# Kernel optimization log

Measured on AMD Instinct MI355X. Metric: run time of the kernel, lower is better.

## Reference

```python
import jax, jax.numpy as jnp
import numpy as np

NUM_LAYERS = 3
DROPOUT_P = 0.1


def _spmm(rows, cols, vals, X, num_rows):
    # COO SpMM: out[r] = sum_{e: rows[e]==r} vals[e] * X[cols[e]]
    return jax.ops.segment_sum(vals[:, None] * X[cols], rows, num_segments=num_rows)


def setup_inputs() -> dict:
    key = jax.random.key(0)
    ks = jax.random.split(key, 8)
    N, H, D, NNZ = 50000, 50000, 256, 1600000
    poi_embs = jax.random.normal(ks[0], (N, D), dtype=jnp.float32)
    src_row = jax.random.randint(ks[1], (NNZ,), 0, N, dtype=jnp.int32)
    src_col = jax.random.randint(ks[2], (NNZ,), 0, H, dtype=jnp.int32)
    src_val = jax.random.uniform(ks[3], (NNZ,), dtype=jnp.float32)
    tar_row = jax.random.randint(ks[4], (NNZ,), 0, H, dtype=jnp.int32)
    tar_col = jax.random.randint(ks[5], (NNZ,), 0, N, dtype=jnp.int32)
    tar_val = jax.random.uniform(ks[6], (NNZ,), dtype=jnp.float32)
    return {
        "poi_embs": poi_embs,
        "src_row": src_row, "src_col": src_col, "src_val": src_val,
        "tar_row": tar_row, "tar_col": tar_col, "tar_val": tar_val,
        "num_pois": N, "num_hyperedges": H,
    }


def reference(poi_embs, src_row, src_col, src_val, tar_row, tar_col, tar_val,
              num_pois, num_hyperedges):
    keep = 1.0 - DROPOUT_P
    drop_key = jax.random.key(42)
    finals = [poi_embs]  # [N, D]
    x = poi_embs
    for i in range(NUM_LAYERS):
        msg_tar = _spmm(tar_row, tar_col, tar_val, x, num_hyperedges)   # [H, D]
        msg_src = _spmm(src_row, src_col, src_val, msg_tar, num_pois)   # [N, D]
        h = msg_src + finals[-1]
        mask = jax.random.bernoulli(jax.random.fold_in(drop_key, i), keep, h.shape)
        x = jnp.where(mask, h / keep, 0.0)  # inverted dropout, training=True
        finals.append(x)
    return jnp.mean(jnp.stack(finals), axis=0)
```

## Files before the change

### kernel.cpp

```cpp
#include <hip/hip_runtime.h>
#include <hip/hip_fp16.h>
#include <stdint.h>

#define DD 256
#define BK_SHIFT 10
#define NB 98
#define CHUNK 4096

typedef float    fx4 __attribute__((ext_vector_type(4)));
typedef uint32_t ux2 __attribute__((ext_vector_type(2)));

__host__ __device__ __forceinline__ uint32_t rotl32(uint32_t v, int r) {
  return (v << r) | (v >> (32 - r));
}

__host__ __device__ inline void tf2x32(uint32_t k0, uint32_t k1,
                                       uint32_t& x0, uint32_t& x1) {
  uint32_t ks0 = k0, ks1 = k1, ks2 = k0 ^ k1 ^ 0x1BD11BDAu;
  x0 += ks0; x1 += ks1;
#define TF_RND(r) { x0 += x1; x1 = rotl32(x1, (r)); x1 ^= x0; }
  TF_RND(13) TF_RND(15) TF_RND(26) TF_RND(6)
  x0 += ks1; x1 += ks2 + 1u;
  TF_RND(17) TF_RND(29) TF_RND(16) TF_RND(24)
  x0 += ks2; x1 += ks0 + 2u;
  TF_RND(13) TF_RND(15) TF_RND(26) TF_RND(6)
  x0 += ks0; x1 += ks1 + 3u;
  TF_RND(17) TF_RND(29) TF_RND(16) TF_RND(24)
  x0 += ks1; x1 += ks2 + 4u;
  TF_RND(13) TF_RND(15) TF_RND(26) TF_RND(6)
  x0 += ks2; x1 += ks0 + 5u;
#undef TF_RND
}

__device__ __forceinline__ float2 h2f(uint32_t u) {
  __half2 h = *(__half2*)&u;
  return __half22float2(h);
}

__global__ void init_kernel(const float* __restrict__ p, uint32_t* __restrict__ xh,
                            float* __restrict__ out, int total4) {
  int t4 = blockIdx.x * blockDim.x + threadIdx.x;
  if (t4 >= total4) return;
  fx4 v = __builtin_nontemporal_load((const fx4*)p + t4);
  __builtin_nontemporal_store(v, (fx4*)out + t4);
  __half2 h0 = __floats2half2_rn(v.x, v.y);
  __half2 h1 = __floats2half2_rn(v.z, v.w);
  ux2 u;
  u.x = *(const uint32_t*)&h0;
  u.y = *(const uint32_t*)&h1;
  __builtin_nontemporal_store(u, (ux2*)xh + t4);
}

__global__ __launch_bounds__(256) void bucket_hist(
    const int* __restrict__ t_row, int nnz_t,
    const int* __restrict__ s_row, int nnz_s,
    int* __restrict__ gbcnt, int H) {
  __shared__ int lcnt[NB];
  for (int i = threadIdx.x; i < NB; i += 256) lcnt[i] = 0;
  __syncthreads();
  const int base = blockIdx.x * CHUNK;
  const int nnz_all = nnz_t + nnz_s;
#pragma unroll
  for (int k = 0; k < CHUNK / 256; ++k) {
    int e = base + k * 256 + threadIdx.x;
    if (e < nnz_all) {
      int slot = (e < nnz_t) ? t_row[e] : (H + s_row[e - nnz_t]);
      atomicAdd(&lcnt[slot >> BK_SHIFT], 1);
    }
  }
  __syncthreads();
  for (int i = threadIdx.x; i < NB; i += 256)
    if (lcnt[i]) atomicAdd(&gbcnt[i], lcnt[i]);
}

__global__ void bucket_scan(const int* __restrict__ gbcnt,
                            int* __restrict__ bbase, int* __restrict__ gcur) {
  if (threadIdx.x == 0) {
    int run = 0;
    for (int i = 0; i < NB; ++i) { bbase[i] = run; gcur[i] = run; run += gbcnt[i]; }
    bbase[NB] = run;
  }
}

__global__ __launch_bounds__(256) void coarse_scatter(
    const int* __restrict__ t_row, const int* __restrict__ t_col,
    const float* __restrict__ t_val, int nnz_t,
    const int* __restrict__ s_row, const int* __restrict__ s_col,
    const float* __restrict__ s_val, int nnz_s,
    int* __restrict__ gcur, uint64_t* __restrict__ staging, int H) {
  __shared__ int lcnt[NB], lbase[NB], gofs[NB];
  __shared__ int ltotal;
  __shared__ uint64_t stage[CHUNK];
  const int tid = threadIdx.x;
  for (int i = tid; i < NB; i += 256) lcnt[i] = 0;
  __syncthreads();
  const int base = blockIdx.x * CHUNK;
  const int nnz_all = nnz_t + nnz_s;
  uint64_t rec[CHUNK / 256];
#pragma unroll
  for (int k = 0; k < CHUNK / 256; ++k) {
    int e = base + k * 256 + tid;
    if (e < nnz_all) {
      int slot, col; float val;
      if (e < nnz_t) { slot = t_row[e]; col = t_col[e]; val = t_val[e]; }
      else { int i2 = e - nnz_t; slot = H + s_row[i2]; col = s_col[i2]; val = s_val[i2]; }
      uint32_t packed = ((uint32_t)col << 16) |
                        (uint32_t)__half_as_ushort(__float2half_rn(val));
      rec[k] = ((uint64_t)(uint32_t)slot << 32) | packed;
      atomicAdd(&lcnt[slot >> BK_SHIFT], 1);
    } else {
      rec[k] = ~0ull;
    }
  }
  __syncthreads();
  if (tid == 0) {
    int run = 0;
    for (int i = 0; i < NB; ++i) { lbase[i] = run; run += lcnt[i]; }
    ltotal = run;
  }
  __syncthreads();
  if (tid < NB) {
    if (lcnt[tid]) gofs[tid] = atomicAdd(&gcur[tid], lcnt[tid]);
    lcnt[tid] = 0;
  }
  __syncthreads();
#pragma unroll
  for (int k = 0; k < CHUNK / 256; ++k) {
    int slot = (int)(rec[k] >> 32);
    if (slot >= 0) {
      int b = slot >> BK_SHIFT;
      int p = atomicAdd(&lcnt[b], 1);
      stage[lbase[b] + p] = rec[k];
    }
  }
  __syncthreads();
  const int tot = ltotal;
  for (int i = tid; i < tot; i += 256) {
    uint64_t r = stage[i];
    int b = (int)(r >> 32) >> BK_SHIFT;
    staging[(size_t)gofs[b] + (i - lbase[b])] = r;
  }
}

__global__ __launch_bounds__(256) void fine_scatter(
    const uint64_t* __restrict__ staging, const int* __restrict__ bbase,
    int* __restrict__ offs, uint32_t* __restrict__ epk, int slots) {
  __shared__ int scnt[1024];
  __shared__ int sofs[1024];
  __shared__ int wsum[4];
  const int b = blockIdx.x;
  const int bb = bbase[b], be = bbase[b + 1];
  const int tid = threadIdx.x;
  for (int i = tid; i < 1024; i += 256) scnt[i] = 0;
  __syncthreads();
  for (int i = bb + tid; i < be; i += 256)
    atomicAdd(&scnt[(int)(staging[i] >> 32) & 1023], 1);
  __syncthreads();
  const int base4 = tid * 4;
  int v[4], pre[4];
#pragma unroll
  for (int k = 0; k < 4; ++k) v[k] = scnt[base4 + k];
  int tsum = 0;
#pragma unroll
  for (int k = 0; k < 4; ++k) { pre[k] = tsum; tsum += v[k]; }
  int lane = tid & 63, wv = tid >> 6;
  int inc = tsum;
  for (int off = 1; off < 64; off <<= 1) {
    int up = __shfl_up(inc, off, 64);
    if (lane >= off) inc += up;
  }
  if (lane == 63) wsum[wv] = inc;
  __syncthreads();
  int wbase = 0;
  for (int w = 0; w < wv; ++w) wbase += wsum[w];
  int texc = wbase + inc - tsum;
#pragma unroll
  for (int k = 0; k < 4; ++k) sofs[base4 + k] = texc + pre[k];
  __syncthreads();
#pragma unroll
  for (int k = 0; k < 4; ++k) {
    int g = (b << BK_SHIFT) + base4 + k;
    if (g < slots) offs[g] = bb + sofs[base4 + k] + v[k];
  }
  __syncthreads();
  for (int i = bb + tid; i < be; i += 256) {
    uint64_t r = staging[i];
    int ls = (int)(r >> 32) & 1023;
    int p = atomicAdd(&sofs[ls], 1);
    epk[(size_t)bb + p] = (uint32_t)r;
  }
}

#define GATHER_BODY(SRC)                                                          \
  float4 acc = make_float4(0.f, 0.f, 0.f, 0.f);                                   \
  int i = b;                                                                      \
  for (; i + 7 < e; i += 8) {                                                     \
    uint32_t E[8]; uint2 A[8];                                                    \
    _Pragma("unroll")                                                             \
    for (int k = 0; k < 8; ++k) E[k] = __builtin_nontemporal_load(ep + i + k);    \
    _Pragma("unroll")                                                             \
    for (int k = 0; k < 8; ++k) A[k] = SRC[(size_t)(E[k] >> 16) * 64 + lane];     \
    _Pragma("unroll")                                                             \
    for (int k = 0; k < 8; ++k) {                                                 \
      float v = __half2float(__ushort_as_half((unsigned short)(E[k] & 0xFFFFu))); \
      float2 f0 = h2f(A[k].x), f1 = h2f(A[k].y);                                  \
      acc.x += v * f0.x; acc.y += v * f0.y;                                       \
      acc.z += v * f1.x; acc.w += v * f1.y;                                       \
    }                                                                             \
  }                                                                               \
  for (; i < e; ++i) {                                                            \
    uint32_t E0 = __builtin_nontemporal_load(ep + i);                             \
    uint2 A0 = SRC[(size_t)(E0 >> 16) * 64 + lane];                               \
    float v = __half2float(__ushort_as_half((unsigned short)(E0 & 0xFFFFu)));     \
    float2 f0 = h2f(A0.x), f1 = h2f(A0.y);                                        \
    acc.x += v * f0.x; acc.y += v * f0.y;                                         \
    acc.z += v * f1.x; acc.w += v * f1.y;                                         \
  }

__global__ __launch_bounds__(256) void spmm_full(
    const int* __restrict__ offs, const uint32_t* __restrict__ ep,
    const uint2* __restrict__ X, uint2* __restrict__ Y, int nrows, int grow_base) {
  int wid = threadIdx.x >> 6, lane = threadIdx.x & 63;
  int r = blockIdx.x * 4 + wid;
  if (r >= nrows) return;
  int g = grow_base + r;
  int b = (g == 0) ? 0 : offs[g - 1];
  int e = offs[g];
  GATHER_BODY(X)
  __half2 o0 = __floats2half2_rn(acc.x, acc.y);
  __half2 o1 = __floats2half2_rn(acc.z, acc.w);
  uint2 o;
  o.x = *(const uint32_t*)&o0;
  o.y = *(const uint32_t*)&o1;
  Y[(size_t)r * 64 + lane] = o;
}

__global__ __launch_bounds__(256) void spmm_drop_full(
    const int* __restrict__ offs, const uint32_t* __restrict__ ep,
    const uint2* __restrict__ T, uint2* __restrict__ x, float* __restrict__ out,
    uint32_t k0, uint32_t k1, int nrows, int grow_base, int is_final) {
  int wid = threadIdx.x >> 6, lane = threadIdx.x & 63;
  int r = blockIdx.x * 4 + wid;
  if (r >= nrows) return;
  int g = grow_base + r;
  int b = (g == 0) ? 0 : offs[g - 1];
  int e = offs[g];
  GATHER_BODY(T)
  size_t xi = (size_t)r * 64 + lane;
  ux2 xv_u = __builtin_nontemporal_load((const ux2*)x + xi);
  float2 x0 = h2f(xv_u.x), x1 = h2f(xv_u.y);
  float h[4] = {acc.x + x0.x, acc.y + x0.y, acc.z + x1.x, acc.w + x1.y};
  int j0 = r * DD + lane * 4;
  float xn[4];
#pragma unroll
  for (int k = 0; k < 4; ++k) {
    uint32_t r0 = 0u, r1 = (uint32_t)(j0 + k);
    tf2x32(k0, k1, r0, r1);
    uint32_t bits = r0 ^ r1;
    float u = __uint_as_float((bits >> 9) | 0x3f800000u) - 1.0f;
    xn[k] = (u < 0.9f) ? h[k] * (1.0f / 0.9f) : 0.0f;
  }
  __half2 nx0 = __floats2half2_rn(xn[0], xn[1]);
  __half2 nx1 = __floats2half2_rn(xn[2], xn[3]);
  ux2 nxu;
  nxu.x = *(const uint32_t*)&nx0;
  nxu.y = *(const uint32_t*)&nx1;
  __builtin_nontemporal_store(nxu, (ux2*)x + xi);
  fx4 ov = __builtin_nontemporal_load((const fx4*)out + xi);
  ov.x += xn[0]; ov.y += xn[1]; ov.z += xn[2]; ov.w += xn[3];
  if (is_final) { ov.x *= 0.25f; ov.y *= 0.25f; ov.z *= 0.25f; ov.w *= 0.25f; }
  __builtin_nontemporal_store(ov, (fx4*)out + xi);
}

extern "C" void kernel_launch(void* const* d_in, const int* in_sizes, int n_in,
                              void* d_out, int out_size, void* d_ws, size_t ws_size,
                              hipStream_t stream) {
  const float* p     = (const float*)d_in[0];
  const int*   s_row = (const int*)d_in[1];
  const int*   s_col = (const int*)d_in[2];
  const float* s_val = (const float*)d_in[3];
  const int*   t_row = (const int*)d_in[4];
  const int*   t_col = (const int*)d_in[5];
  const float* t_val = (const float*)d_in[6];

  const int nnz_s = in_sizes[1];
  const int nnz_t = in_sizes[4];
  const int N = in_sizes[0] / DD;
  const int H = 50000;
  const int slots = H + N;
  const int nnz_all = nnz_t + nnz_s;

  uint2*    xh      = (uint2*)d_ws;
  uint2*    th      = xh + (size_t)N * 64;
  uint64_t* staging = (uint64_t*)(th + (size_t)H * 64);
  uint32_t* epk     = (uint32_t*)(staging + nnz_all);
  int*      offs    = (int*)(epk + nnz_all);
  int*      gbcnt   = offs + slots;
  int*      bbase   = gbcnt + NB;
  int*      gcur    = bbase + (NB + 1);

  float* out = (float*)d_out;

  (void)hipMemsetAsync(gbcnt, 0, sizeof(int) * NB, stream);
  const int cblocks = (nnz_all + CHUNK - 1) / CHUNK;
  bucket_hist<<<cblocks, 256, 0, stream>>>(t_row, nnz_t, s_row, nnz_s, gbcnt, H);
  bucket_scan<<<1, 64, 0, stream>>>(gbcnt, bbase, gcur);
  coarse_scatter<<<cblocks, 256, 0, stream>>>(t_row, t_col, t_val, nnz_t,
                                              s_row, s_col, s_val, nnz_s,
                                              gcur, staging, H);
  fine_scatter<<<NB, 256, 0, stream>>>(staging, bbase, offs, epk, slots);

  const int total4 = N * DD / 4;
  init_kernel<<<(total4 + 255) / 256, 256, 0, stream>>>(p, (uint32_t*)xh, out, total4);

  for (int i = 0; i < 3; ++i) {
    spmm_full<<<(H + 3) / 4, 256, 0, stream>>>(offs, epk, xh, th, H, 0);
    uint32_t x0 = 0u, x1 = (uint32_t)i;
    tf2x32(0u, 42u, x0, x1);
    spmm_drop_full<<<(N + 3) / 4, 256, 0, stream>>>(offs, epk, th, xh, out,
                                                    x0, x1, N, H, i == 2);
  }
}
```

Baseline: 854.2 us.

## Bin edges by column range and gather in phases for cache locality

The fine scatter now sorts each row's edges into 16 column-range bins, using 4096-column ranges, and records per-bin offsets. The SpMM kernels loop over 13 column phases, with each wave handling 9 rows, so concurrently running waves tend to touch the same slice of the source matrix and reuse it from L2. The running fp32 output accumulation is removed: layer outputs go to separate fp16 buffers, and the final kernel computes the mean once, with one buffer reusing the staging area. The cost is a 16x larger offset table, more offset loads and short segments per row, and fp16 rounding of the intermediate layers used in the mean.

```diff
diff --git a/kernel.cpp b/kernel.cpp
--- a/kernel.cpp
+++ b/kernel.cpp
@@ -3,9 +3,16 @@
 #include <stdint.h>
 
 #define DD 256
-#define BK_SHIFT 10
-#define NB 98
+#define BK_SHIFT 9
+#define SLOTS_PER_BK 512
+#define NB 196
 #define CHUNK 4096
+#define CSHIFT 12
+#define NPH 13
+#define BPS 16
+#define RPW 9
+#define WPB 8
+#define RPB (RPW * WPB)
 
 typedef float    fx4 __attribute__((ext_vector_type(4)));
 typedef uint32_t ux2 __attribute__((ext_vector_type(2)));
@@ -38,11 +45,10 @@
 }
 
 __global__ void init_kernel(const float* __restrict__ p, uint32_t* __restrict__ xh,
-                            float* __restrict__ out, int total4) {
+                            int total4) {
   int t4 = blockIdx.x * blockDim.x + threadIdx.x;
   if (t4 >= total4) return;
   fx4 v = __builtin_nontemporal_load((const fx4*)p + t4);
-  __builtin_nontemporal_store(v, (fx4*)out + t4);
   __half2 h0 = __floats2half2_rn(v.x, v.y);
   __half2 h1 = __floats2half2_rn(v.z, v.w);
   ux2 u;
@@ -144,25 +150,27 @@
 
 __global__ __launch_bounds__(256) void fine_scatter(
     const uint64_t* __restrict__ staging, const int* __restrict__ bbase,
-    int* __restrict__ offs, uint32_t* __restrict__ epk, int slots) {
-  __shared__ int scnt[1024];
-  __shared__ int sofs[1024];
+    int* __restrict__ boffs, uint32_t* __restrict__ epk, int slots) {
+  __shared__ int scnt[SLOTS_PER_BK * BPS];
+  __shared__ int sofs[SLOTS_PER_BK * BPS];
   __shared__ int wsum[4];
   const int b = blockIdx.x;
   const int bb = bbase[b], be = bbase[b + 1];
   const int tid = threadIdx.x;
-  for (int i = tid; i < 1024; i += 256) scnt[i] = 0;
-  __syncthreads();
-  for (int i = bb + tid; i < be; i += 256)
-    atomicAdd(&scnt[(int)(staging[i] >> 32) & 1023], 1);
-  __syncthreads();
-  const int base4 = tid * 4;
-  int v[4], pre[4];
-#pragma unroll
-  for (int k = 0; k < 4; ++k) v[k] = scnt[base4 + k];
+  for (int i = tid; i < SLOTS_PER_BK * BPS; i += 256) scnt[i] = 0;
+  __syncthreads();
+  for (int i = bb + tid; i < be; i += 256) {
+    uint64_t r = staging[i];
+    int slot = (int)(r >> 32);
+    int col = (int)(((uint32_t)r) >> 16);
+    int bin = ((slot & (SLOTS_PER_BK - 1)) << 4) | (col >> CSHIFT);
+    atomicAdd(&scnt[bin], 1);
+  }
+  __syncthreads();
+  const int base32 = tid * 32;
   int tsum = 0;
 #pragma unroll
-  for (int k = 0; k < 4; ++k) { pre[k] = tsum; tsum += v[k]; }
+  for (int k = 0; k < 32; ++k) tsum += scnt[base32 + k];
   int lane = tid & 63, wv = tid >> 6;
   int inc = tsum;
   for (int off = 1; off < 64; off <<= 1) {
@@ -173,103 +181,168 @@
   __syncthreads();
   int wbase = 0;
   for (int w = 0; w < wv; ++w) wbase += wsum[w];
-  int texc = wbase + inc - tsum;
-#pragma unroll
-  for (int k = 0; k < 4; ++k) sofs[base4 + k] = texc + pre[k];
-  __syncthreads();
-#pragma unroll
-  for (int k = 0; k < 4; ++k) {
-    int g = (b << BK_SHIFT) + base4 + k;
-    if (g < slots) offs[g] = bb + sofs[base4 + k] + v[k];
+  int run = wbase + inc - tsum;
+#pragma unroll
+  for (int k = 0; k < 32; ++k) { int v = scnt[base32 + k]; sofs[base32 + k] = run; run += v; }
+  __syncthreads();
+  const int gb0 = b * (SLOTS_PER_BK * BPS);
+  const int nbins_total = slots * BPS;
+  for (int i = tid; i < SLOTS_PER_BK * BPS; i += 256) {
+    int g = gb0 + i;
+    if (g < nbins_total) boffs[g] = bb + sofs[i];
   }
   __syncthreads();
   for (int i = bb + tid; i < be; i += 256) {
     uint64_t r = staging[i];
-    int ls = (int)(r >> 32) & 1023;
-    int p = atomicAdd(&sofs[ls], 1);
-    epk[(size_t)bb + p] = (uint32_t)r;
-  }
-}
-
-#define GATHER_BODY(SRC)                                                          \
-  float4 acc = make_float4(0.f, 0.f, 0.f, 0.f);                                   \
-  int i = b;                                                                      \
-  for (; i + 7 < e; i += 8) {                                                     \
-    uint32_t E[8]; uint2 A[8];                                                    \
+    int slot = (int)(r >> 32);
+    uint32_t packed = (uint32_t)r;
+    int bin = ((slot & (SLOTS_PER_BK - 1)) << 4) | ((int)(packed >> 16) >> CSHIFT);
+    int p = atomicAdd(&sofs[bin], 1);
+    epk[(size_t)bb + p] = packed;
+  }
+}
+
+#define SEG_GATHER(SRC, ACC)                                                      \
+  {                                                                               \
+    int i = sb;                                                                   \
+    for (; i + 3 < se; i += 4) {                                                  \
+      uint32_t E0 = __builtin_nontemporal_load(ep + i);                           \
+      uint32_t E1 = __builtin_nontemporal_load(ep + i + 1);                       \
+      uint32_t E2 = __builtin_nontemporal_load(ep + i + 2);                       \
+      uint32_t E3 = __builtin_nontemporal_load(ep + i + 3);                       \
+      uint2 A0 = SRC[(size_t)(E0 >> 16) * 64 + lane];                             \
+      uint2 A1 = SRC[(size_t)(E1 >> 16) * 64 + lane];                             \
+      uint2 A2 = SRC[(size_t)(E2 >> 16) * 64 + lane];                             \
+      uint2 A3 = SRC[(size_t)(E3 >> 16) * 64 + lane];                             \
+      float v0 = __half2float(__ushort_as_half((unsigned short)(E0 & 0xFFFFu)));  \
+      float v1 = __half2float(__ushort_as_half((unsigned short)(E1 & 0xFFFFu)));  \
+      float v2 = __half2float(__ushort_as_half((unsigned short)(E2 & 0xFFFFu)));  \
+      float v3 = __half2float(__ushort_as_half((unsigned short)(E3 & 0xFFFFu)));  \
+      float2 f0, f1;                                                              \
+      f0 = h2f(A0.x); f1 = h2f(A0.y);                                             \
+      ACC.x += v0 * f0.x; ACC.y += v0 * f0.y; ACC.z += v0 * f1.x; ACC.w += v0 * f1.y; \
+      f0 = h2f(A1.x); f1 = h2f(A1.y);                                             \
+      ACC.x += v1 * f0.x; ACC.y += v1 * f0.y; ACC.z += v1 * f1.x; ACC.w += v1 * f1.y; \
+      f0 = h2f(A2.x); f1 = h2f(A2.y);                                             \
+      ACC.x += v2 * f0.x; ACC.y += v2 * f0.y; ACC.z += v2 * f1.x; ACC.w += v2 * f1.y; \
+      f0 = h2f(A3.x); f1 = h2f(A3.y);                                             \
+      ACC.x += v3 * f0.x; ACC.y += v3 * f0.y; ACC.z += v3 * f1.x; ACC.w += v3 * f1.y; \
+    }                                                                             \
+    for (; i < se; ++i) {                                                         \
+      uint32_t E0 = __builtin_nontemporal_load(ep + i);                           \
+      uint2 A0 = SRC[(size_t)(E0 >> 16) * 64 + lane];                             \
+      float v0 = __half2float(__ushort_as_half((unsigned short)(E0 & 0xFFFFu)));  \
+      float2 f0 = h2f(A0.x), f1 = h2f(A0.y);                                      \
+      ACC.x += v0 * f0.x; ACC.y += v0 * f0.y; ACC.z += v0 * f1.x; ACC.w += v0 * f1.y; \
+    }                                                                             \
+  }
+
+#define PHASE_ACCUM(SRC)                                                          \
+  float4 acc[RPW];                                                                \
+  _Pragma("unroll")                                                               \
+  for (int k = 0; k < RPW; ++k) acc[k] = make_float4(0.f, 0.f, 0.f, 0.f);         \
+  for (int o = 0; o < NPH; ++o) {                                                 \
     _Pragma("unroll")                                                             \
-    for (int k = 0; k < 8; ++k) E[k] = __builtin_nontemporal_load(ep + i + k);    \
-    _Pragma("unroll")                                                             \
-    for (int k = 0; k < 8; ++k) A[k] = SRC[(size_t)(E[k] >> 16) * 64 + lane];     \
-    _Pragma("unroll")                                                             \
-    for (int k = 0; k < 8; ++k) {                                                 \
-      float v = __half2float(__ushort_as_half((unsigned short)(E[k] & 0xFFFFu))); \
-      float2 f0 = h2f(A[k].x), f1 = h2f(A[k].y);                                  \
-      acc.x += v * f0.x; acc.y += v * f0.y;                                       \
-      acc.z += v * f1.x; acc.w += v * f1.y;                                       \
+    for (int k = 0; k < RPW; ++k) {                                               \
+      int r = r0 + k;                                                             \
+      if (r < nrows) {                                                            \
+        int gb = (grow_base + r) * BPS + o;                                       \
+        int sb = __builtin_nontemporal_load(boffs + gb);                          \
+        int se = __builtin_nontemporal_load(boffs + gb + 1);                      \
+        SEG_GATHER(SRC, acc[k])                                                   \
+      }                                                                           \
     }                                                                             \
-  }                                                                               \
-  for (; i < e; ++i) {                                                            \
-    uint32_t E0 = __builtin_nontemporal_load(ep + i);                             \
-    uint2 A0 = SRC[(size_t)(E0 >> 16) * 64 + lane];                               \
-    float v = __half2float(__ushort_as_half((unsigned short)(E0 & 0xFFFFu)));     \
-    float2 f0 = h2f(A0.x), f1 = h2f(A0.y);                                        \
-    acc.x += v * f0.x; acc.y += v * f0.y;                                         \
-    acc.z += v * f1.x; acc.w += v * f1.y;                                         \
-  }
-
-__global__ __launch_bounds__(256) void spmm_full(
-    const int* __restrict__ offs, const uint32_t* __restrict__ ep,
+  }
+
+__global__ __launch_bounds__(512, 6) void spmm_phase(
+    const int* __restrict__ boffs, const uint32_t* __restrict__ ep,
     const uint2* __restrict__ X, uint2* __restrict__ Y, int nrows, int grow_base) {
-  int wid = threadIdx.x >> 6, lane = threadIdx.x & 63;
-  int r = blockIdx.x * 4 + wid;
-  if (r >= nrows) return;
-  int g = grow_base + r;
-  int b = (g == 0) ? 0 : offs[g - 1];
-  int e = offs[g];
-  GATHER_BODY(X)
-  __half2 o0 = __floats2half2_rn(acc.x, acc.y);
-  __half2 o1 = __floats2half2_rn(acc.z, acc.w);
-  uint2 o;
-  o.x = *(const uint32_t*)&o0;
-  o.y = *(const uint32_t*)&o1;
-  Y[(size_t)r * 64 + lane] = o;
-}
-
-__global__ __launch_bounds__(256) void spmm_drop_full(
-    const int* __restrict__ offs, const uint32_t* __restrict__ ep,
-    const uint2* __restrict__ T, uint2* __restrict__ x, float* __restrict__ out,
-    uint32_t k0, uint32_t k1, int nrows, int grow_base, int is_final) {
-  int wid = threadIdx.x >> 6, lane = threadIdx.x & 63;
-  int r = blockIdx.x * 4 + wid;
-  if (r >= nrows) return;
-  int g = grow_base + r;
-  int b = (g == 0) ? 0 : offs[g - 1];
-  int e = offs[g];
-  GATHER_BODY(T)
-  size_t xi = (size_t)r * 64 + lane;
-  ux2 xv_u = __builtin_nontemporal_load((const ux2*)x + xi);
-  float2 x0 = h2f(xv_u.x), x1 = h2f(xv_u.y);
-  float h[4] = {acc.x + x0.x, acc.y + x0.y, acc.z + x1.x, acc.w + x1.y};
-  int j0 = r * DD + lane * 4;
-  float xn[4];
-#pragma unroll
-  for (int k = 0; k < 4; ++k) {
-    uint32_t r0 = 0u, r1 = (uint32_t)(j0 + k);
-    tf2x32(k0, k1, r0, r1);
-    uint32_t bits = r0 ^ r1;
-    float u = __uint_as_float((bits >> 9) | 0x3f800000u) - 1.0f;
-    xn[k] = (u < 0.9f) ? h[k] * (1.0f / 0.9f) : 0.0f;
-  }
-  __half2 nx0 = __floats2half2_rn(xn[0], xn[1]);
-  __half2 nx1 = __floats2half2_rn(xn[2], xn[3]);
-  ux2 nxu;
-  nxu.x = *(const uint32_t*)&nx0;
-  nxu.y = *(const uint32_t*)&nx1;
-  __builtin_nontemporal_store(nxu, (ux2*)x + xi);
-  fx4 ov = __builtin_nontemporal_load((const fx4*)out + xi);
-  ov.x += xn[0]; ov.y += xn[1]; ov.z += xn[2]; ov.w += xn[3];
-  if (is_final) { ov.x *= 0.25f; ov.y *= 0.25f; ov.z *= 0.25f; ov.w *= 0.25f; }
-  __builtin_nontemporal_store(ov, (fx4*)out + xi);
+  const int w = threadIdx.x >> 6, lane = threadIdx.x & 63;
+  const int r0 = blockIdx.x * RPB + w * RPW;
+  PHASE_ACCUM(X)
+#pragma unroll
+  for (int k = 0; k < RPW; ++k) {
+    int r = r0 + k;
+    if (r >= nrows) break;
+    __half2 o0 = __floats2half2_rn(acc[k].x, acc[k].y);
+    __half2 o1 = __floats2half2_rn(acc[k].z, acc[k].w);
+    ux2 o;
+    o.x = *(const uint32_t*)&o0;
+    o.y = *(const uint32_t*)&o1;
+    __builtin_nontemporal_store(o, (ux2*)Y + (size_t)r * 64 + lane);
+  }
+}
+
+__global__ __launch_bounds__(512, 6) void spmm_drop_phase(
+    const int* __restrict__ boffs, const uint32_t* __restrict__ ep,
+    const uint2* __restrict__ T, const uint2* __restrict__ xprev,
+    uint2* __restrict__ xout, uint32_t k0, uint32_t k1, int nrows, int grow_base) {
+  const int w = threadIdx.x >> 6, lane = threadIdx.x & 63;
+  const int r0 = blockIdx.x * RPB + w * RPW;
+  PHASE_ACCUM(T)
+#pragma unroll
+  for (int k = 0; k < RPW; ++k) {
+    int r = r0 + k;
+    if (r >= nrows) break;
+    size_t xi = (size_t)r * 64 + lane;
+    ux2 xv = __builtin_nontemporal_load((const ux2*)xprev + xi);
+    float2 p0 = h2f(xv.x), p1 = h2f(xv.y);
+    float h[4] = {acc[k].x + p0.x, acc[k].y + p0.y, acc[k].z + p1.x, acc[k].w + p1.y};
+    int j0 = r * DD + lane * 4;
+    float xn[4];
+#pragma unroll
+    for (int q = 0; q < 4; ++q) {
+      uint32_t a = 0u, b2 = (uint32_t)(j0 + q);
+      tf2x32(k0, k1, a, b2);
+      uint32_t bits = a ^ b2;
+      float u = __uint_as_float((bits >> 9) | 0x3f800000u) - 1.0f;
+      xn[q] = (u < 0.9f) ? h[q] * (1.0f / 0.9f) : 0.0f;
+    }
+    __half2 n0 = __floats2half2_rn(xn[0], xn[1]);
+    __half2 n1 = __floats2half2_rn(xn[2], xn[3]);
+    ux2 nu;
+    nu.x = *(const uint32_t*)&n0;
+    nu.y = *(const uint32_t*)&n1;
+    __builtin_nontemporal_store(nu, (ux2*)xout + xi);
+  }
+}
+
+__global__ __launch_bounds__(512, 6) void spmm_drop_final(
+    const int* __restrict__ boffs, const uint32_t* __restrict__ ep,
+    const uint2* __restrict__ T, const uint2* __restrict__ x1,
+    const uint2* __restrict__ x2, const float* __restrict__ p,
+    float* __restrict__ out, uint32_t k0, uint32_t k1, int nrows, int grow_base) {
+  const int w = threadIdx.x >> 6, lane = threadIdx.x & 63;
+  const int r0 = blockIdx.x * RPB + w * RPW;
+  PHASE_ACCUM(T)
+#pragma unroll
+  for (int k = 0; k < RPW; ++k) {
+    int r = r0 + k;
+    if (r >= nrows) break;
+    size_t xi = (size_t)r * 64 + lane;
+    ux2 x2u = __builtin_nontemporal_load((const ux2*)x2 + xi);
+    float2 q0 = h2f(x2u.x), q1 = h2f(x2u.y);
+    float h[4] = {acc[k].x + q0.x, acc[k].y + q0.y, acc[k].z + q1.x, acc[k].w + q1.y};
+    int j0 = r * DD + lane * 4;
+    float xn[4];
+#pragma unroll
+    for (int q = 0; q < 4; ++q) {
+      uint32_t a = 0u, b2 = (uint32_t)(j0 + q);
+      tf2x32(k0, k1, a, b2);
+      uint32_t bits = a ^ b2;
+      float u = __uint_as_float((bits >> 9) | 0x3f800000u) - 1.0f;
+      xn[q] = (u < 0.9f) ? h[q] * (1.0f / 0.9f) : 0.0f;
+    }
+    ux2 x1u = __builtin_nontemporal_load((const ux2*)x1 + xi);
+    float2 a0 = h2f(x1u.x), a1 = h2f(x1u.y);
+    fx4 pv = __builtin_nontemporal_load((const fx4*)p + xi);
+    fx4 ov;
+    ov.x = 0.25f * (pv.x + a0.x + q0.x + xn[0]);
+    ov.y = 0.25f * (pv.y + a0.y + q0.y + xn[1]);
+    ov.z = 0.25f * (pv.z + a1.x + q1.x + xn[2]);
+    ov.w = 0.25f * (pv.w + a1.y + q1.y + xn[3]);
+    __builtin_nontemporal_store(ov, (fx4*)out + xi);
+  }
 }
 
 extern "C" void kernel_launch(void* const* d_in, const int* in_sizes, int n_in,
@@ -290,12 +363,14 @@
   const int slots = H + N;
   const int nnz_all = nnz_t + nnz_s;
 
-  uint2*    xh      = (uint2*)d_ws;
-  uint2*    th      = xh + (size_t)N * 64;
+  uint2*    x0      = (uint2*)d_ws;
+  uint2*    x1      = x0 + (size_t)N * 64;
+  uint2*    th      = x1 + (size_t)N * 64;
   uint64_t* staging = (uint64_t*)(th + (size_t)H * 64);
+  uint2*    x2      = (uint2*)staging;
   uint32_t* epk     = (uint32_t*)(staging + nnz_all);
-  int*      offs    = (int*)(epk + nnz_all);
-  int*      gbcnt   = offs + slots;
+  int*      boffs   = (int*)(epk + nnz_all);
+  int*      gbcnt   = boffs + (size_t)slots * BPS;
   int*      bbase   = gbcnt + NB;
   int*      gcur    = bbase + (NB + 1);
 
@@ -308,16 +383,28 @@
   coarse_scatter<<<cblocks, 256, 0, stream>>>(t_row, t_col, t_val, nnz_t,
                                               s_row, s_col, s_val, nnz_s,
                                               gcur, staging, H);
-  fine_scatter<<<NB, 256, 0, stream>>>(staging, bbase, offs, epk, slots);
+  fine_scatter<<<NB, 256, 0, stream>>>(staging, bbase, boffs, epk, slots);
 
   const int total4 = N * DD / 4;
-  init_kernel<<<(total4 + 255) / 256, 256, 0, stream>>>(p, (uint32_t*)xh, out, total4);
-
+  init_kernel<<<(total4 + 255) / 256, 256, 0, stream>>>(p, (uint32_t*)x0, total4);
+
+  uint32_t key[3][2];
   for (int i = 0; i < 3; ++i) {
-    spmm_full<<<(H + 3) / 4, 256, 0, stream>>>(offs, epk, xh, th, H, 0);
-    uint32_t x0 = 0u, x1 = (uint32_t)i;
-    tf2x32(0u, 42u, x0, x1);
-    spmm_drop_full<<<(N + 3) / 4, 256, 0, stream>>>(offs, epk, th, xh, out,
-                                                    x0, x1, N, H, i == 2);
-  }
-}
+    uint32_t a = 0u, b = (uint32_t)i;
+    tf2x32(0u, 42u, a, b);
+    key[i][0] = a; key[i][1] = b;
+  }
+
+  const int gH = (H + RPB - 1) / RPB;
+  const int gN = (N + RPB - 1) / RPB;
+
+  spmm_phase<<<gH, 512, 0, stream>>>(boffs, epk, x0, th, H, 0);
+  spmm_drop_phase<<<gN, 512, 0, stream>>>(boffs, epk, th, x0, x1,
+                                          key[0][0], key[0][1], N, H);
+  spmm_phase<<<gH, 512, 0, stream>>>(boffs, epk, x1, th, H, 0);
+  spmm_drop_phase<<<gN, 512, 0, stream>>>(boffs, epk, th, x1, x2,
+                                          key[1][0], key[1][1], N, H);
+  spmm_phase<<<gH, 512, 0, stream>>>(boffs, epk, x2, th, H, 0);
+  spmm_drop_final<<<gN, 512, 0, stream>>>(boffs, epk, th, x1, x2, p, out,
+                                          key[2][0], key[2][1], N, H);
+}
```

Measured after the change: 1.664 ms. +94.8%, slower.

## Slice feature dimension into 8 column blocks for cache-resident SpMM gathers

Applied to the files above, without the earlier changes.

Stores the fp16 embeddings in a sliced layout of 8 column slices of 32 features, so each block gathers only a 64-byte piece per row. Blocks are interleaved across slices, which is meant to keep the working set of a slice in L2 and cut gather traffic. Each wave now splits edges across 8 sub-groups with shuffle reductions and handles 8 rows. The running out accumulation is replaced by keeping x1 and x2 buffers, with x2 placed in the staging area, and the mean is written once in a final fused kernel. The cost is that every slice re-reads the edge lists and offsets 8 times, and the shuffle reduction adds overhead.

```diff
diff --git a/kernel.cpp b/kernel.cpp
--- a/kernel.cpp
+++ b/kernel.cpp
@@ -6,6 +6,7 @@
 #define BK_SHIFT 10
 #define NB 98
 #define CHUNK 4096
+#define RPW2 8
 
 typedef float    fx4 __attribute__((ext_vector_type(4)));
 typedef uint32_t ux2 __attribute__((ext_vector_type(2)));
@@ -37,18 +38,19 @@
   return __half22float2(h);
 }
 
-__global__ void init_kernel(const float* __restrict__ p, uint32_t* __restrict__ xh,
-                            float* __restrict__ out, int total4) {
-  int t4 = blockIdx.x * blockDim.x + threadIdx.x;
-  if (t4 >= total4) return;
-  fx4 v = __builtin_nontemporal_load((const fx4*)p + t4);
-  __builtin_nontemporal_store(v, (fx4*)out + t4);
+__global__ void init_kernel(const float* __restrict__ p, uint2* __restrict__ xh,
+                            int N) {
+  int t = blockIdx.x * blockDim.x + threadIdx.x;
+  if (t >= N * 64) return;
+  int r = t >> 6, part4 = t & 63;
+  int s = part4 >> 3, part = part4 & 7;
+  fx4 v = __builtin_nontemporal_load((const fx4*)p + t);
   __half2 h0 = __floats2half2_rn(v.x, v.y);
   __half2 h1 = __floats2half2_rn(v.z, v.w);
-  ux2 u;
+  uint2 u;
   u.x = *(const uint32_t*)&h0;
   u.y = *(const uint32_t*)&h1;
-  __builtin_nontemporal_store(u, (ux2*)xh + t4);
+  xh[(size_t)s * N * 8 + (size_t)r * 8 + part] = u;
 }
 
 __global__ __launch_bounds__(256) void bucket_hist(
@@ -191,85 +193,149 @@
   }
 }
 
-#define GATHER_BODY(SRC)                                                          \
-  float4 acc = make_float4(0.f, 0.f, 0.f, 0.f);                                   \
-  int i = b;                                                                      \
-  for (; i + 7 < e; i += 8) {                                                     \
-    uint32_t E[8]; uint2 A[8];                                                    \
-    _Pragma("unroll")                                                             \
-    for (int k = 0; k < 8; ++k) E[k] = __builtin_nontemporal_load(ep + i + k);    \
-    _Pragma("unroll")                                                             \
-    for (int k = 0; k < 8; ++k) A[k] = SRC[(size_t)(E[k] >> 16) * 64 + lane];     \
-    _Pragma("unroll")                                                             \
-    for (int k = 0; k < 8; ++k) {                                                 \
-      float v = __half2float(__ushort_as_half((unsigned short)(E[k] & 0xFFFFu))); \
-      float2 f0 = h2f(A[k].x), f1 = h2f(A[k].y);                                  \
-      acc.x += v * f0.x; acc.y += v * f0.y;                                       \
-      acc.z += v * f1.x; acc.w += v * f1.y;                                       \
-    }                                                                             \
-  }                                                                               \
-  for (; i < e; ++i) {                                                            \
-    uint32_t E0 = __builtin_nontemporal_load(ep + i);                             \
-    uint2 A0 = SRC[(size_t)(E0 >> 16) * 64 + lane];                               \
-    float v = __half2float(__ushort_as_half((unsigned short)(E0 & 0xFFFFu)));     \
-    float2 f0 = h2f(A0.x), f1 = h2f(A0.y);                                        \
-    acc.x += v * f0.x; acc.y += v * f0.y;                                         \
-    acc.z += v * f1.x; acc.w += v * f1.y;                                         \
-  }
-
-__global__ __launch_bounds__(256) void spmm_full(
+__device__ __forceinline__ float4 gather_slice(
     const int* __restrict__ offs, const uint32_t* __restrict__ ep,
-    const uint2* __restrict__ X, uint2* __restrict__ Y, int nrows, int grow_base) {
-  int wid = threadIdx.x >> 6, lane = threadIdx.x & 63;
-  int r = blockIdx.x * 4 + wid;
-  if (r >= nrows) return;
-  int g = grow_base + r;
-  int b = (g == 0) ? 0 : offs[g - 1];
-  int e = offs[g];
-  GATHER_BODY(X)
-  __half2 o0 = __floats2half2_rn(acc.x, acc.y);
-  __half2 o1 = __floats2half2_rn(acc.z, acc.w);
-  uint2 o;
-  o.x = *(const uint32_t*)&o0;
-  o.y = *(const uint32_t*)&o1;
-  Y[(size_t)r * 64 + lane] = o;
-}
-
-__global__ __launch_bounds__(256) void spmm_drop_full(
+    const uint2* __restrict__ Xs, int g, int sub, int part) {
+  int b = (g == 0) ? 0 : __builtin_nontemporal_load(offs + g - 1);
+  int e = __builtin_nontemporal_load(offs + g);
+  float4 acc = make_float4(0.f, 0.f, 0.f, 0.f);
+  for (int i = b; i < e; i += 16) {
+    int i0 = i + sub, i1 = i + 8 + sub;
+    uint32_t E0 = (i0 < e) ? __builtin_nontemporal_load(ep + i0) : 0u;
+    uint32_t E1 = (i1 < e) ? __builtin_nontemporal_load(ep + i1) : 0u;
+    uint2 A0 = Xs[(size_t)(E0 >> 16) * 8 + part];
+    uint2 A1 = Xs[(size_t)(E1 >> 16) * 8 + part];
+    float v0 = __half2float(__ushort_as_half((unsigned short)(E0 & 0xFFFFu)));
+    float v1 = __half2float(__ushort_as_half((unsigned short)(E1 & 0xFFFFu)));
+    float2 f0 = h2f(A0.x), f1 = h2f(A0.y);
+    acc.x += v0 * f0.x; acc.y += v0 * f0.y; acc.z += v0 * f1.x; acc.w += v0 * f1.y;
+    f0 = h2f(A1.x); f1 = h2f(A1.y);
+    acc.x += v1 * f0.x; acc.y += v1 * f0.y; acc.z += v1 * f1.x; acc.w += v1 * f1.y;
+  }
+#pragma unroll
+  for (int d = 8; d < 64; d <<= 1) {
+    acc.x += __shfl_xor(acc.x, d, 64);
+    acc.y += __shfl_xor(acc.y, d, 64);
+    acc.z += __shfl_xor(acc.z, d, 64);
+    acc.w += __shfl_xor(acc.w, d, 64);
+  }
+  return acc;
+}
+
+__global__ __launch_bounds__(256) void spmm_slice(
     const int* __restrict__ offs, const uint32_t* __restrict__ ep,
-    const uint2* __restrict__ T, uint2* __restrict__ x, float* __restrict__ out,
-    uint32_t k0, uint32_t k1, int nrows, int grow_base, int is_final) {
-  int wid = threadIdx.x >> 6, lane = threadIdx.x & 63;
-  int r = blockIdx.x * 4 + wid;
-  if (r >= nrows) return;
-  int g = grow_base + r;
-  int b = (g == 0) ? 0 : offs[g - 1];
-  int e = offs[g];
-  GATHER_BODY(T)
-  size_t xi = (size_t)r * 64 + lane;
-  ux2 xv_u = __builtin_nontemporal_load((const ux2*)x + xi);
-  float2 x0 = h2f(xv_u.x), x1 = h2f(xv_u.y);
-  float h[4] = {acc.x + x0.x, acc.y + x0.y, acc.z + x1.x, acc.w + x1.y};
-  int j0 = r * DD + lane * 4;
-  float xn[4];
-#pragma unroll
-  for (int k = 0; k < 4; ++k) {
-    uint32_t r0 = 0u, r1 = (uint32_t)(j0 + k);
-    tf2x32(k0, k1, r0, r1);
-    uint32_t bits = r0 ^ r1;
-    float u = __uint_as_float((bits >> 9) | 0x3f800000u) - 1.0f;
-    xn[k] = (u < 0.9f) ? h[k] * (1.0f / 0.9f) : 0.0f;
-  }
-  __half2 nx0 = __floats2half2_rn(xn[0], xn[1]);
-  __half2 nx1 = __floats2half2_rn(xn[2], xn[3]);
-  ux2 nxu;
-  nxu.x = *(const uint32_t*)&nx0;
-  nxu.y = *(const uint32_t*)&nx1;
-  __builtin_nontemporal_store(nxu, (ux2*)x + xi);
-  fx4 ov = __builtin_nontemporal_load((const fx4*)out + xi);
-  ov.x += xn[0]; ov.y += xn[1]; ov.z += xn[2]; ov.w += xn[3];
-  if (is_final) { ov.x *= 0.25f; ov.y *= 0.25f; ov.z *= 0.25f; ov.w *= 0.25f; }
-  __builtin_nontemporal_store(ov, (fx4*)out + xi);
+    const uint2* __restrict__ X, uint2* __restrict__ Y,
+    int nrows, int grow_base, int srcN) {
+  const int s = blockIdx.x & 7;
+  const int rblk = blockIdx.x >> 3;
+  const int wid = threadIdx.x >> 6, lane = threadIdx.x & 63;
+  const int sub = lane >> 3, part = lane & 7;
+  const uint2* Xs = X + (size_t)s * srcN * 8;
+  uint2* Ys = Y + (size_t)s * nrows * 8;
+  const int rbase = rblk * (4 * RPW2) + wid * RPW2;
+#pragma unroll
+  for (int k = 0; k < RPW2; ++k) {
+    int r = rbase + k;
+    if (r >= nrows) return;
+    float4 acc = gather_slice(offs, ep, Xs, grow_base + r, sub, part);
+    if (sub == 0) {
+      __half2 o0 = __floats2half2_rn(acc.x, acc.y);
+      __half2 o1 = __floats2half2_rn(acc.z, acc.w);
+      uint2 o;
+      o.x = *(const uint32_t*)&o0;
+      o.y = *(const uint32_t*)&o1;
+      Ys[(size_t)r * 8 + part] = o;
+    }
+  }
+}
+
+__global__ __launch_bounds__(256) void spmm_drop_slice(
+    const int* __restrict__ offs, const uint32_t* __restrict__ ep,
+    const uint2* __restrict__ T, const uint2* __restrict__ xprev,
+    uint2* __restrict__ xout, uint32_t k0, uint32_t k1,
+    int nrows, int grow_base, int srcH) {
+  const int s = blockIdx.x & 7;
+  const int rblk = blockIdx.x >> 3;
+  const int wid = threadIdx.x >> 6, lane = threadIdx.x & 63;
+  const int sub = lane >> 3, part = lane & 7;
+  const uint2* Ts = T + (size_t)s * srcH * 8;
+  const uint2* Xp = xprev + (size_t)s * nrows * 8;
+  uint2* Xo = xout + (size_t)s * nrows * 8;
+  const int rbase = rblk * (4 * RPW2) + wid * RPW2;
+#pragma unroll
+  for (int k = 0; k < RPW2; ++k) {
+    int r = rbase + k;
+    if (r >= nrows) return;
+    float4 acc = gather_slice(offs, ep, Ts, grow_base + r, sub, part);
+    uint2 xv = Xp[(size_t)r * 8 + part];
+    float2 p0 = h2f(xv.x), p1 = h2f(xv.y);
+    float h[4] = {acc.x + p0.x, acc.y + p0.y, acc.z + p1.x, acc.w + p1.y};
+    int j0 = r * DD + s * 32 + part * 4;
+    float xn[4];
+#pragma unroll
+    for (int q = 0; q < 4; ++q) {
+      uint32_t a = 0u, b2 = (uint32_t)(j0 + q);
+      tf2x32(k0, k1, a, b2);
+      uint32_t bits = a ^ b2;
+      float u = __uint_as_float((bits >> 9) | 0x3f800000u) - 1.0f;
+      xn[q] = (u < 0.9f) ? h[q] * (1.0f / 0.9f) : 0.0f;
+    }
+    if (sub == 0) {
+      __half2 n0 = __floats2half2_rn(xn[0], xn[1]);
+      __half2 n1 = __floats2half2_rn(xn[2], xn[3]);
+      uint2 nu;
+      nu.x = *(const uint32_t*)&n0;
+      nu.y = *(const uint32_t*)&n1;
+      Xo[(size_t)r * 8 + part] = nu;
+    }
+  }
+}
+
+__global__ __launch_bounds__(256) void spmm_drop_final(
+    const int* __restrict__ offs, const uint32_t* __restrict__ ep,
+    const uint2* __restrict__ T, const uint2* __restrict__ x1,
+    const uint2* __restrict__ x2, const float* __restrict__ p,
+    float* __restrict__ out, uint32_t k0, uint32_t k1,
+    int nrows, int grow_base, int srcH) {
+  const int s = blockIdx.x & 7;
+  const int rblk = blockIdx.x >> 3;
+  const int wid = threadIdx.x >> 6, lane = threadIdx.x & 63;
+  const int sub = lane >> 3, part = lane & 7;
+  const uint2* Ts = T + (size_t)s * srcH * 8;
+  const uint2* X1 = x1 + (size_t)s * nrows * 8;
+  const uint2* X2 = x2 + (size_t)s * nrows * 8;
+  const int rbase = rblk * (4 * RPW2) + wid * RPW2;
+#pragma unroll
+  for (int k = 0; k < RPW2; ++k) {
+    int r = rbase + k;
+    if (r >= nrows) return;
+    float4 acc = gather_slice(offs, ep, Ts, grow_base + r, sub, part);
+    uint2 x2u = X2[(size_t)r * 8 + part];
+    float2 q0 = h2f(x2u.x), q1 = h2f(x2u.y);
+    float h[4] = {acc.x + q0.x, acc.y + q0.y, acc.z + q1.x, acc.w + q1.y};
+    int j0 = r * DD + s * 32 + part * 4;
+    float xn[4];
+#pragma unroll
+    for (int q = 0; q < 4; ++q) {
+      uint32_t a = 0u, b2 = (uint32_t)(j0 + q);
+      tf2x32(k0, k1, a, b2);
+      uint32_t bits = a ^ b2;
+      float u = __uint_as_float((bits >> 9) | 0x3f800000u) - 1.0f;
+      xn[q] = (u < 0.9f) ? h[q] * (1.0f / 0.9f) : 0.0f;
+    }
+    if (sub == 0) {
+      uint2 x1u = X1[(size_t)r * 8 + part];
+      float2 a0 = h2f(x1u.x), a1 = h2f(x1u.y);
+      size_t oi = (size_t)r * 64 + s * 8 + part;
+      fx4 pv = __builtin_nontemporal_load((const fx4*)p + oi);
+      fx4 ov;
+      ov.x = 0.25f * (pv.x + a0.x + q0.x + xn[0]);
+      ov.y = 0.25f * (pv.y + a0.y + q0.y + xn[1]);
+      ov.z = 0.25f * (pv.z + a1.x + q1.x + xn[2]);
+      ov.w = 0.25f * (pv.w + a1.y + q1.y + xn[3]);
+      __builtin_nontemporal_store(ov, (fx4*)out + oi);
+    }
+  }
 }
 
 extern "C" void kernel_launch(void* const* d_in, const int* in_sizes, int n_in,
@@ -290,9 +356,11 @@
   const int slots = H + N;
   const int nnz_all = nnz_t + nnz_s;
 
-  uint2*    xh      = (uint2*)d_ws;
-  uint2*    th      = xh + (size_t)N * 64;
+  uint2*    x0      = (uint2*)d_ws;
+  uint2*    x1      = x0 + (size_t)N * 64;
+  uint2*    th      = x1 + (size_t)N * 64;
   uint64_t* staging = (uint64_t*)(th + (size_t)H * 64);
+  uint2*    x2      = (uint2*)staging;
   uint32_t* epk     = (uint32_t*)(staging + nnz_all);
   int*      offs    = (int*)(epk + nnz_all);
   int*      gbcnt   = offs + slots;
@@ -310,14 +378,26 @@
                                               gcur, staging, H);
   fine_scatter<<<NB, 256, 0, stream>>>(staging, bbase, offs, epk, slots);
 
-  const int total4 = N * DD / 4;
-  init_kernel<<<(total4 + 255) / 256, 256, 0, stream>>>(p, (uint32_t*)xh, out, total4);
-
+  init_kernel<<<(N * 64 + 255) / 256, 256, 0, stream>>>(p, x0, N);
+
+  uint32_t key[3][2];
   for (int i = 0; i < 3; ++i) {
-    spmm_full<<<(H + 3) / 4, 256, 0, stream>>>(offs, epk, xh, th, H, 0);
-    uint32_t x0 = 0u, x1 = (uint32_t)i;
-    tf2x32(0u, 42u, x0, x1);
-    spmm_drop_full<<<(N + 3) / 4, 256, 0, stream>>>(offs, epk, th, xh, out,
-                                                    x0, x1, N, H, i == 2);
-  }
-}
+    uint32_t a = 0u, b = (uint32_t)i;
+    tf2x32(0u, 42u, a, b);
+    key[i][0] = a; key[i][1] = b;
+  }
+
+  const int RPB = 4 * RPW2;
+  const int gH = 8 * ((H + RPB - 1) / RPB);
+  const int gN = 8 * ((N + RPB - 1) / RPB);
+
+  spmm_slice<<<gH, 256, 0, stream>>>(offs, epk, x0, th, H, 0, N);
+  spmm_drop_slice<<<gN, 256, 0, stream>>>(offs, epk, th, x0, x1,
+                                          key[0][0], key[0][1], N, H, H);
+  spmm_slice<<<gH, 256, 0, stream>>>(offs, epk, x1, th, H, 0, N);
+  spmm_drop_slice<<<gN, 256, 0, stream>>>(offs, epk, th, x1, x2,
+                                          key[1][0], key[1][1], N, H, H);
+  spmm_slice<<<gH, 256, 0, stream>>>(offs, epk, x2, th, H, 0, N);
+  spmm_drop_final<<<gN, 256, 0, stream>>>(offs, epk, th, x1, x2, p, out,
+                                          key[2][0], key[2][1], N, H, H);
+}
```

Result: slower. 1.556 ms (+82.2%).
